# Optimization experiments

Hardware: AMD Instinct MI355X
Metric: run time of the kernel (lower is better)

## Reference

```python
import jax, jax.numpy as jnp
import numpy as np

DEPTH = 6


def sparsemax(z):
    # sparsemax along last axis (matches tfa.activations.sparsemax default axis=-1)
    d = z.shape[-1]
    z_sorted = -jnp.sort(-z, axis=-1)                      # descending
    cs = jnp.cumsum(z_sorted, axis=-1)
    k = jnp.arange(1, d + 1, dtype=z.dtype)
    support = z_sorted * k > (cs - 1.0)
    k_sup = jnp.sum(support, axis=-1, keepdims=True)       # size of support
    cs_k = jnp.take_along_axis(cs, k_sup.astype(jnp.int32) - 1, axis=-1)
    tau = (cs_k - 1.0) / k_sup.astype(z.dtype)
    return jnp.maximum(z - tau, 0.0)


def binary_lut(depth):
    # (depth, 2^depth, 2): bit s of each leaf code and its complement
    idx = jnp.arange(2 ** depth)
    off = 2 ** jnp.arange(depth)
    bits = (idx[None, :] // off[:, None]) % 2
    return jnp.stack([bits, 1 - bits], axis=-1).astype(jnp.float32)


def setup_inputs() -> dict:
    key = jax.random.key(0)
    ks = jax.random.split(key, 5)
    batch, dim, n_trees, depth, units = 1024, 256, 512, DEPTH, 16
    return {
        "x": jax.random.normal(ks[0], (batch, dim), dtype=jnp.float32),
        "feature_selection_logits": jax.random.normal(ks[1], (dim, n_trees, depth), dtype=jnp.float32),
        "feature_thresholds": jax.random.normal(ks[2], (n_trees, depth), dtype=jnp.float32) * 0.1,
        "log_temperatures": jax.random.normal(ks[3], (n_trees, depth), dtype=jnp.float32) * 0.1,
        "response": jax.random.normal(ks[4], (n_trees, units, 2 ** depth), dtype=jnp.float32),
    }


def reference(x, feature_selection_logits, feature_thresholds, log_temperatures, response):
    lut = binary_lut(DEPTH)                                     # (d, c, 2)
    selectors = sparsemax(feature_selection_logits)             # (i, n, d)
    fv = jnp.einsum('bi,ind->bnd', x, selectors)                # (b, n, d)
    tl = (fv - feature_thresholds) * jnp.exp(-log_temperatures) # (b, n, d)
    tl2 = jnp.stack([-tl, tl], axis=-1)                         # (b, n, d, 2)
    gates = jnp.clip(0.5 * tl2 + 0.5, 0.0, 1.0)                 # sparsemoid
    rg = jnp.einsum('bnds,dcs->bndc', gates, lut)               # (b, n, d, 2^d)
    rg = jnp.prod(rg, axis=-2)                                  # (b, n, 2^d)
    out = jnp.einsum('bnc,nuc->bnu', rg, response)              # (b, n, u)
    return jnp.mean(out, axis=1)                                # (b, u)
```

## Files before the change

kernel.cpp:

```cpp
#include <hip/hip_runtime.h>
#include <hip/hip_bf16.h>

#define DEPTH   6
#define NLEAF   64
#define BATCH   1024
#define DIM     256
#define NTREES  512
#define UNITS   16

#define BTILE   128
#define TTILE   8
#define KCHUNK  32
#define NTILES  (NTREES / TTILE)
#define BBLK    (BATCH / BTILE)
#define NDCOLS  (TTILE * DEPTH)

#define WS_SELP    0
#define WS_INVTEMP (WS_SELP + DIM*NTREES*DEPTH)
#define WS_THRP    (WS_INVTEMP + NTREES*DEPTH)
#define WS_PARTIAL (WS_THRP + NTREES*DEPTH)

__global__ void prep_small(const float* __restrict__ thr,
                           const float* __restrict__ lt,
                           float* __restrict__ invtemp,
                           float* __restrict__ thrp) {
    int i = blockIdx.x * 256 + threadIdx.x;
    if (i < NTREES * DEPTH) {
        float it = __expf(-lt[i]);
        invtemp[i] = it;
        thrp[i]    = thr[i] * it;
    }
}

__global__ void prep_sparsemax(const float* __restrict__ fsl,
                               const float* __restrict__ invtemp,
                               float* __restrict__ selp) {
    int t = blockIdx.x * 256 + threadIdx.x;
    int i = t >> 9;
    int n = t & (NTREES - 1);
    int base = (i * NTREES + n) * DEPTH;

    float zv[DEPTH], zs[DEPTH];
#pragma unroll
    for (int d = 0; d < DEPTH; ++d) { zv[d] = fsl[base + d]; zs[d] = zv[d]; }

#pragma unroll
    for (int p = 0; p < DEPTH - 1; ++p) {
#pragma unroll
        for (int j = 0; j < DEPTH - 1 - p; ++j) {
            float a = zs[j], b = zs[j + 1];
            zs[j]     = fmaxf(a, b);
            zs[j + 1] = fminf(a, b);
        }
    }

    float cs[DEPTH];
    cs[0] = zs[0];
#pragma unroll
    for (int d = 1; d < DEPTH; ++d) cs[d] = cs[d - 1] + zs[d];

    int k = 0;
#pragma unroll
    for (int d = 0; d < DEPTH; ++d)
        if (zs[d] * (float)(d + 1) > cs[d] - 1.0f) k++;

    float csk = cs[0];
#pragma unroll
    for (int d = 0; d < DEPTH; ++d) csk = (k - 1 == d) ? cs[d] : csk;

    float tau = (csk - 1.0f) / (float)k;

#pragma unroll
    for (int d = 0; d < DEPTH; ++d) {
        float it = invtemp[n * DEPTH + d];
        selp[base + d] = fmaxf(zv[d] - tau, 0.0f) * it;
    }
}

__global__ __launch_bounds__(256)
void main_kernel(const float* __restrict__ x,
                 const float* __restrict__ selp,
                 const float* __restrict__ thrp,
                 const float* __restrict__ resp,
                 float* __restrict__ partial) {
    __shared__ union SM {
        struct {
            float x[KCHUNK][132];
            float sel[KCHUNK][TTILE * 8];
        } a;
        float gates[NDCOLS][BTILE];
    } sm;

    const int tid   = threadIdx.x;
    const int ntile = blockIdx.x;
    const int btile = blockIdx.y;
    const int b0    = btile * BTILE;
    const int col0  = ntile * NDCOLS;
    const int ng0   = ntile * TTILE;

    const int tn = tid & (TTILE - 1);
    const int tb = tid >> 3;

    float acc[4][DEPTH];
#pragma unroll
    for (int bb = 0; bb < 4; ++bb)
#pragma unroll
        for (int d = 0; d < DEPTH; ++d) acc[bb][d] = 0.0f;

    for (int kc = 0; kc < DIM; kc += KCHUNK) {
#pragma unroll
        for (int i = 0; i < 16; ++i) {
            int e = tid + i * 256;
            int b = e >> 5;
            int k = e & 31;
            sm.a.x[k][b] = x[(b0 + b) * DIM + kc + k];
        }
#pragma unroll
        for (int i = 0; i < 6; ++i) {
            int e = tid + i * 256;
            int k = e / NDCOLS;
            int c = e - k * NDCOLS;
            int tt = c / DEPTH;
            int d  = c - tt * DEPTH;
            sm.a.sel[k][tt * 8 + d] = selp[(kc + k) * (NTREES * DEPTH) + col0 + c];
        }
        __syncthreads();

#pragma unroll 8
        for (int k = 0; k < KCHUNK; ++k) {
            float4 xv = *(const float4*)&sm.a.x[k][tb * 4];
            float4 s0 = *(const float4*)&sm.a.sel[k][tn * 8];
            float2 s1 = *(const float2*)&sm.a.sel[k][tn * 8 + 4];
            float xb[4] = {xv.x, xv.y, xv.z, xv.w};
            float sv[DEPTH] = {s0.x, s0.y, s0.z, s0.w, s1.x, s1.y};
#pragma unroll
            for (int bb = 0; bb < 4; ++bb)
#pragma unroll
                for (int d = 0; d < DEPTH; ++d)
                    acc[bb][d] = fmaf(xb[bb], sv[d], acc[bb][d]);
        }
        __syncthreads();
    }

#pragma unroll
    for (int d = 0; d < DEPTH; ++d) {
        float th = thrp[(ng0 + tn) * DEPTH + d];
#pragma unroll
        for (int bb = 0; bb < 4; ++bb) {
            float tl = acc[bb][d] - th;
            float g  = fminf(fmaxf(0.5f * tl + 0.5f, 0.0f), 1.0f);
            sm.gates[tn * DEPTH + d][tb * 4 + bb] = g;
        }
    }
    __syncthreads();

    const int b  = tid & (BTILE - 1);
    const int uh = __builtin_amdgcn_readfirstlane(tid >> 7);

    float out8[8];
#pragma unroll
    for (int u = 0; u < 8; ++u) out8[u] = 0.0f;

    for (int n = 0; n < TTILE; ++n) {
        float g[DEPTH];
#pragma unroll
        for (int d = 0; d < DEPTH; ++d) g[d] = sm.gates[n * DEPTH + d][b];

        float p[NLEAF];
        p[0] = 1.0f;
#pragma unroll
        for (int d = 0; d < DEPTH; ++d) {
            int w = 1 << d;
            float gd = g[d], hd = 1.0f - g[d];
#pragma unroll
            for (int c = w - 1; c >= 0; --c) {
                float base = p[c];
                p[c + w] = base * hd;
                p[c]     = base * gd;
            }
        }

        const float* rp = resp + (((ng0 + n) * UNITS) + uh * 8) * NLEAF;
#pragma unroll
        for (int u = 0; u < 8; ++u) {
            float a = 0.0f;
#pragma unroll
            for (int c = 0; c < NLEAF; ++c)
                a = fmaf(p[c], rp[u * NLEAF + c], a);
            out8[u] += a;
        }
    }

    float* pp = partial + ((size_t)(ntile * BATCH + b0 + b)) * UNITS + uh * 8;
    float4 w0 = {out8[0], out8[1], out8[2], out8[3]};
    float4 w1 = {out8[4], out8[5], out8[6], out8[7]};
    *(float4*)&pp[0] = w0;
    *(float4*)&pp[4] = w1;
}

__global__ void reduce_kernel(const float* __restrict__ partial,
                              float* __restrict__ out) {
    int idx = blockIdx.x * 256 + threadIdx.x;
    float s = 0.0f;
#pragma unroll 8
    for (int nt = 0; nt < NTILES; ++nt)
        s += partial[(size_t)nt * BATCH * UNITS + idx];
    out[idx] = s * (1.0f / (float)NTREES);
}

extern "C" void kernel_launch(void* const* d_in, const int* in_sizes, int n_in,
                              void* d_out, int out_size, void* d_ws, size_t ws_size,
                              hipStream_t stream) {
    const float* x    = (const float*)d_in[0];
    const float* fsl  = (const float*)d_in[1];
    const float* thr  = (const float*)d_in[2];
    const float* lt   = (const float*)d_in[3];
    const float* resp = (const float*)d_in[4];
    float* out = (float*)d_out;
    float* ws  = (float*)d_ws;

    float* selp    = ws + WS_SELP;
    float* invtemp = ws + WS_INVTEMP;
    float* thrp    = ws + WS_THRP;
    float* partial = ws + WS_PARTIAL;

    prep_small<<<(NTREES * DEPTH + 255) / 256, 256, 0, stream>>>(thr, lt, invtemp, thrp);
    prep_sparsemax<<<(DIM * NTREES) / 256, 256, 0, stream>>>(fsl, invtemp, selp);
    main_kernel<<<dim3(NTILES, BBLK), 256, 0, stream>>>(x, selp, thrp, resp, partial);
    reduce_kernel<<<(BATCH * UNITS) / 256, 256, 0, stream>>>(partial, out);
}
```

Measured before the change: 158.6 us.

## Split fused kernel into register-tiled GEMM for gates and separate tree kernel

Replaces the fused GEMM-plus-tree kernel with a dedicated 64x64 register-tiled GEMM that writes gates to a global buffer, followed by a tree kernel that processes four trees per thread straight from those gates. It also merges the two prep kernels into one and aliases the selector buffer with the partial-sum buffer. The aim is better GEMM efficiency and occupancy than the shared-memory-limited fused design, paid for by a 12 MB gates round-trip through global memory. The old fused path is kept as a fallback when the workspace is too small.

New measurement: 232.4 us. +46.5%, slower.

```diff
diff --git a/kernel.cpp b/kernel.cpp
--- a/kernel.cpp
+++ b/kernel.cpp
@@ -7,52 +7,59 @@
 #define DIM     256
 #define NTREES  512
 #define UNITS   16
-
-#define BTILE   128
-#define TTILE   8
-#define KCHUNK  32
-#define NTILES  (NTREES / TTILE)
-#define BBLK    (BATCH / BTILE)
-#define NDCOLS  (TTILE * DEPTH)
-
-#define WS_SELP    0
-#define WS_INVTEMP (WS_SELP + DIM*NTREES*DEPTH)
-#define WS_THRP    (WS_INVTEMP + NTREES*DEPTH)
-#define WS_PARTIAL (WS_THRP + NTREES*DEPTH)
-
-__global__ void prep_small(const float* __restrict__ thr,
-                           const float* __restrict__ lt,
-                           float* __restrict__ invtemp,
-                           float* __restrict__ thrp) {
-    int i = blockIdx.x * 256 + threadIdx.x;
-    if (i < NTREES * DEPTH) {
-        float it = __expf(-lt[i]);
-        invtemp[i] = it;
-        thrp[i]    = thr[i] * it;
-    }
-}
-
-__global__ void prep_sparsemax(const float* __restrict__ fsl,
-                               const float* __restrict__ invtemp,
-                               float* __restrict__ selp) {
+#define NCOLS   (NTREES*DEPTH)
+
+#define TM    64
+#define TN    64
+#define KCH   32
+#define APAD  36
+#define BPAD  68
+#define MB    (BATCH/TM)
+#define NB    (NCOLS/TN)
+
+#define TPT   4
+#define NTG   (NTREES/TPT)
+
+#define WS_GATES 0
+#define WS_THRP  (WS_GATES + BATCH*NCOLS)
+#define WS_SH    (WS_THRP + NCOLS)
+#define WS_PRIMARY_FLOATS (WS_SH + NTG*BATCH*UNITS)
+
+#define FB_SELP    0
+#define FB_THRP    (FB_SELP + DIM*NTREES*DEPTH)
+#define FB_PARTIAL (FB_THRP + NCOLS)
+#define FBT   8
+#define FBB   128
+#define FBK   32
+#define FBNT  (NTREES/FBT)
+#define FBBB  (BATCH/FBB)
+#define FBND  (FBT*DEPTH)
+
+__global__ void prep_kernel(const float* __restrict__ fsl,
+                            const float* __restrict__ thr,
+                            const float* __restrict__ lt,
+                            float* __restrict__ selp,
+                            float* __restrict__ thrp) {
+    if (blockIdx.x == (DIM * NTREES) / 256) {
+        for (int j = threadIdx.x; j < NCOLS; j += 256)
+            thrp[j] = thr[j] * __expf(-lt[j]);
+        return;
+    }
     int t = blockIdx.x * 256 + threadIdx.x;
-    int i = t >> 9;
     int n = t & (NTREES - 1);
-    int base = (i * NTREES + n) * DEPTH;
+    int base = t * DEPTH;
 
     float zv[DEPTH], zs[DEPTH];
 #pragma unroll
     for (int d = 0; d < DEPTH; ++d) { zv[d] = fsl[base + d]; zs[d] = zv[d]; }
 
 #pragma unroll
-    for (int p = 0; p < DEPTH - 1; ++p) {
+    for (int p = 0; p < DEPTH - 1; ++p)
 #pragma unroll
         for (int j = 0; j < DEPTH - 1 - p; ++j) {
             float a = zs[j], b = zs[j + 1];
-            zs[j]     = fmaxf(a, b);
-            zs[j + 1] = fminf(a, b);
-        }
-    }
+            zs[j] = fmaxf(a, b); zs[j + 1] = fminf(a, b);
+        }
 
     float cs[DEPTH];
     cs[0] = zs[0];
@@ -67,38 +74,196 @@
     float csk = cs[0];
 #pragma unroll
     for (int d = 0; d < DEPTH; ++d) csk = (k - 1 == d) ? cs[d] : csk;
-
     float tau = (csk - 1.0f) / (float)k;
 
 #pragma unroll
     for (int d = 0; d < DEPTH; ++d) {
-        float it = invtemp[n * DEPTH + d];
+        float it = __expf(-lt[n * DEPTH + d]);
         selp[base + d] = fmaxf(zv[d] - tau, 0.0f) * it;
     }
 }
 
+__global__ __launch_bounds__(128)
+void gemm_gates(const float* __restrict__ x,
+                const float* __restrict__ selp,
+                const float* __restrict__ thrp,
+                float* __restrict__ gates) {
+    __shared__ float la[TM * APAD];
+    __shared__ float lb[KCH * BPAD];
+
+    const int tid = threadIdx.x;
+    const int n0  = blockIdx.x * TN;
+    const int m0  = blockIdx.y * TM;
+    const int tx  = tid & 7;
+    const int ty  = tid >> 3;
+
+    float acc[4][8];
+#pragma unroll
+    for (int r = 0; r < 4; ++r)
+#pragma unroll
+        for (int c = 0; c < 8; ++c) acc[r][c] = 0.0f;
+
+    float4 ra[4], rb[4];
+    int ar[4], ak[4], bk[4], bc_[4];
+#pragma unroll
+    for (int i = 0; i < 4; ++i) {
+        int e = tid + i * 128;
+        ar[i] = e >> 3;  ak[i] = e & 7;
+        bk[i] = e >> 4;  bc_[i] = e & 15;
+    }
+
+#define STAGE(KC_)                                                            \
+    _Pragma("unroll")                                                         \
+    for (int i = 0; i < 4; ++i) {                                             \
+        ra[i] = *(const float4*)&x[(m0 + ar[i]) * DIM + (KC_) * KCH + ak[i] * 4]; \
+        rb[i] = *(const float4*)&selp[((KC_) * KCH + bk[i]) * NCOLS + n0 + bc_[i] * 4]; \
+    }
+#define COMMIT()                                                              \
+    _Pragma("unroll")                                                         \
+    for (int i = 0; i < 4; ++i) {                                             \
+        *(float4*)&la[ar[i] * APAD + ak[i] * 4] = ra[i];                      \
+        *(float4*)&lb[bk[i] * BPAD + bc_[i] * 4] = rb[i];                     \
+    }
+
+    STAGE(0)
+    COMMIT()
+    __syncthreads();
+
+    const int NKC = DIM / KCH;
+    for (int kc = 0; kc < NKC; ++kc) {
+        if (kc < NKC - 1) STAGE(kc + 1)
+
+#pragma unroll
+        for (int kk = 0; kk < KCH; kk += 4) {
+            float a4[4][4];
+#pragma unroll
+            for (int r = 0; r < 4; ++r)
+                *(float4*)a4[r] = *(const float4*)&la[(ty * 4 + r) * APAD + kk];
+            float b4[4][8];
+#pragma unroll
+            for (int j = 0; j < 4; ++j) {
+                *(float4*)&b4[j][0] = *(const float4*)&lb[(kk + j) * BPAD + tx * 8];
+                *(float4*)&b4[j][4] = *(const float4*)&lb[(kk + j) * BPAD + tx * 8 + 4];
+            }
+#pragma unroll
+            for (int j = 0; j < 4; ++j)
+#pragma unroll
+                for (int r = 0; r < 4; ++r)
+#pragma unroll
+                    for (int c = 0; c < 8; ++c)
+                        acc[r][c] = fmaf(a4[r][j], b4[j][c], acc[r][c]);
+        }
+
+        if (kc < NKC - 1) {
+            __syncthreads();
+            COMMIT()
+            __syncthreads();
+        }
+    }
+#undef STAGE
+#undef COMMIT
+
+    float th[8];
+    *(float4*)&th[0] = *(const float4*)&thrp[n0 + tx * 8];
+    *(float4*)&th[4] = *(const float4*)&thrp[n0 + tx * 8 + 4];
+#pragma unroll
+    for (int r = 0; r < 4; ++r) {
+        float o[8];
+#pragma unroll
+        for (int c = 0; c < 8; ++c) {
+            float tl = acc[r][c] - th[c];
+            o[c] = fminf(fmaxf(fmaf(0.5f, tl, 0.5f), 0.0f), 1.0f);
+        }
+        float* gp = &gates[(size_t)(m0 + ty * 4 + r) * NCOLS + n0 + tx * 8];
+        *(float4*)&gp[0] = *(float4*)&o[0];
+        *(float4*)&gp[4] = *(float4*)&o[4];
+    }
+}
+
 __global__ __launch_bounds__(256)
-void main_kernel(const float* __restrict__ x,
-                 const float* __restrict__ selp,
-                 const float* __restrict__ thrp,
+void tree_kernel(const float* __restrict__ gates,
                  const float* __restrict__ resp,
                  float* __restrict__ partial) {
+    const int bid  = blockIdx.x;
+    const int bc   = bid & 7;
+    const int tg   = bid >> 3;
+    const int tid  = threadIdx.x;
+    const int lane = tid & 63;
+    const int uh   = __builtin_amdgcn_readfirstlane((tid >> 6) & 1);
+    const int b    = bc * 128 + (tid >> 7) * 64 + lane;
+
+    float g[TPT * DEPTH];
+    const float* gp = gates + (size_t)b * NCOLS + tg * (TPT * DEPTH);
+#pragma unroll
+    for (int i = 0; i < 6; ++i)
+        *(float4*)&g[i * 4] = *(const float4*)&gp[i * 4];
+
+    float out8[8];
+#pragma unroll
+    for (int u = 0; u < 8; ++u) out8[u] = 0.0f;
+
+#pragma unroll
+    for (int t = 0; t < TPT; ++t) {
+        float p[NLEAF];
+        p[0] = 1.0f;
+#pragma unroll
+        for (int d = 0; d < DEPTH; ++d) {
+            int w = 1 << d;
+            float gd = g[t * DEPTH + d], hd = 1.0f - gd;
+#pragma unroll
+            for (int c = w - 1; c >= 0; --c) {
+                float base = p[c];
+                p[c + w] = base * hd;
+                p[c]     = base * gd;
+            }
+        }
+        const float* rp = resp + (size_t)((tg * TPT + t) * UNITS + uh * 8) * NLEAF;
+#pragma unroll
+        for (int u = 0; u < 8; ++u) {
+            float a = 0.0f;
+#pragma unroll
+            for (int c = 0; c < NLEAF; ++c)
+                a = fmaf(p[c], rp[u * NLEAF + c], a);
+            out8[u] += a;
+        }
+    }
+
+    float* pp = partial + ((size_t)tg * BATCH + b) * UNITS + uh * 8;
+    *(float4*)&pp[0] = *(float4*)&out8[0];
+    *(float4*)&pp[4] = *(float4*)&out8[4];
+}
+
+__global__ void reduce_kernel(const float* __restrict__ partial,
+                              float* __restrict__ out, int nt) {
+    int idx = blockIdx.x * 256 + threadIdx.x;
+    float s = 0.0f;
+    for (int tg = 0; tg < nt; ++tg)
+        s += partial[(size_t)tg * BATCH * UNITS + idx];
+    out[idx] = s * (1.0f / (float)NTREES);
+}
+
+__global__ __launch_bounds__(256)
+void fused_kernel(const float* __restrict__ x,
+                  const float* __restrict__ selp,
+                  const float* __restrict__ thrp,
+                  const float* __restrict__ resp,
+                  float* __restrict__ partial) {
     __shared__ union SM {
         struct {
-            float x[KCHUNK][132];
-            float sel[KCHUNK][TTILE * 8];
+            float x[FBK][132];
+            float sel[FBK][FBT * 8];
         } a;
-        float gates[NDCOLS][BTILE];
+        float gates[FBND][FBB];
     } sm;
 
     const int tid   = threadIdx.x;
     const int ntile = blockIdx.x;
     const int btile = blockIdx.y;
-    const int b0    = btile * BTILE;
-    const int col0  = ntile * NDCOLS;
-    const int ng0   = ntile * TTILE;
-
-    const int tn = tid & (TTILE - 1);
+    const int b0    = btile * FBB;
+    const int col0  = ntile * FBND;
+    const int ng0   = ntile * FBT;
+
+    const int tn = tid & (FBT - 1);
     const int tb = tid >> 3;
 
     float acc[4][DEPTH];
@@ -107,7 +272,7 @@
 #pragma unroll
         for (int d = 0; d < DEPTH; ++d) acc[bb][d] = 0.0f;
 
-    for (int kc = 0; kc < DIM; kc += KCHUNK) {
+    for (int kc = 0; kc < DIM; kc += FBK) {
 #pragma unroll
         for (int i = 0; i < 16; ++i) {
             int e = tid + i * 256;
@@ -118,16 +283,16 @@
 #pragma unroll
         for (int i = 0; i < 6; ++i) {
             int e = tid + i * 256;
-            int k = e / NDCOLS;
-            int c = e - k * NDCOLS;
+            int k = e / FBND;
+            int c = e - k * FBND;
             int tt = c / DEPTH;
             int d  = c - tt * DEPTH;
-            sm.a.sel[k][tt * 8 + d] = selp[(kc + k) * (NTREES * DEPTH) + col0 + c];
+            sm.a.sel[k][tt * 8 + d] = selp[(kc + k) * NCOLS + col0 + c];
         }
         __syncthreads();
 
 #pragma unroll 8
-        for (int k = 0; k < KCHUNK; ++k) {
+        for (int k = 0; k < FBK; ++k) {
             float4 xv = *(const float4*)&sm.a.x[k][tb * 4];
             float4 s0 = *(const float4*)&sm.a.sel[k][tn * 8];
             float2 s1 = *(const float2*)&sm.a.sel[k][tn * 8 + 4];
@@ -154,14 +319,14 @@
     }
     __syncthreads();
 
-    const int b  = tid & (BTILE - 1);
+    const int b  = tid & (FBB - 1);
     const int uh = __builtin_amdgcn_readfirstlane(tid >> 7);
 
     float out8[8];
 #pragma unroll
     for (int u = 0; u < 8; ++u) out8[u] = 0.0f;
 
-    for (int n = 0; n < TTILE; ++n) {
+    for (int n = 0; n < FBT; ++n) {
         float g[DEPTH];
 #pragma unroll
         for (int d = 0; d < DEPTH; ++d) g[d] = sm.gates[n * DEPTH + d][b];
@@ -192,20 +357,8 @@
     }
 
     float* pp = partial + ((size_t)(ntile * BATCH + b0 + b)) * UNITS + uh * 8;
-    float4 w0 = {out8[0], out8[1], out8[2], out8[3]};
-    float4 w1 = {out8[4], out8[5], out8[6], out8[7]};
-    *(float4*)&pp[0] = w0;
-    *(float4*)&pp[4] = w1;
-}
-
-__global__ void reduce_kernel(const float* __restrict__ partial,
-                              float* __restrict__ out) {
-    int idx = blockIdx.x * 256 + threadIdx.x;
-    float s = 0.0f;
-#pragma unroll 8
-    for (int nt = 0; nt < NTILES; ++nt)
-        s += partial[(size_t)nt * BATCH * UNITS + idx];
-    out[idx] = s * (1.0f / (float)NTREES);
+    *(float4*)&pp[0] = *(float4*)&out8[0];
+    *(float4*)&pp[4] = *(float4*)&out8[4];
 }
 
 extern "C" void kernel_launch(void* const* d_in, const int* in_sizes, int n_in,
@@ -219,13 +372,23 @@
     float* out = (float*)d_out;
     float* ws  = (float*)d_ws;
 
-    float* selp    = ws + WS_SELP;
-    float* invtemp = ws + WS_INVTEMP;
-    float* thrp    = ws + WS_THRP;
-    float* partial = ws + WS_PARTIAL;
-
-    prep_small<<<(NTREES * DEPTH + 255) / 256, 256, 0, stream>>>(thr, lt, invtemp, thrp);
-    prep_sparsemax<<<(DIM * NTREES) / 256, 256, 0, stream>>>(fsl, invtemp, selp);
-    main_kernel<<<dim3(NTILES, BBLK), 256, 0, stream>>>(x, selp, thrp, resp, partial);
-    reduce_kernel<<<(BATCH * UNITS) / 256, 256, 0, stream>>>(partial, out);
-}
+    if (ws_size >= (size_t)WS_PRIMARY_FLOATS * sizeof(float)) {
+        float* gates   = ws + WS_GATES;
+        float* thrp    = ws + WS_THRP;
+        float* selp    = ws + WS_SH;
+        float* partial = ws + WS_SH;
+
+        prep_kernel<<<(DIM * NTREES) / 256 + 1, 256, 0, stream>>>(fsl, thr, lt, selp, thrp);
+        gemm_gates<<<dim3(NB, MB), 128, 0, stream>>>(x, selp, thrp, gates);
+        tree_kernel<<<NTG * 8, 256, 0, stream>>>(gates, resp, partial);
+        reduce_kernel<<<(BATCH * UNITS) / 256, 256, 0, stream>>>(partial, out, NTG);
+    } else {
+        float* selp    = ws + FB_SELP;
+        float* thrp    = ws + FB_THRP;
+        float* partial = ws + FB_PARTIAL;
+
+        prep_kernel<<<(DIM * NTREES) / 256 + 1, 256, 0, stream>>>(fsl, thr, lt, selp, thrp);
+        fused_kernel<<<dim3(FBNT, FBBB), 256, 0, stream>>>(x, selp, thrp, resp, partial);
+        reduce_kernel<<<(BATCH * UNITS) / 256, 256, 0, stream>>>(partial, out, FBNT);
+    }
+}
```

## Split fused tree kernel into double-buffered GEMM for gates plus separate tree kernel

Applied to the files above, without the earlier changes.

Replaces the fused kernel, which did the projection and the tree evaluation together, with a standalone 64x64-tiled GEMM that uses double-buffered shared memory and float4 loads. That GEMM writes clipped gates to a workspace buffer, and a separate tree kernel then reads those gates straight from global memory. The intent is a more efficient GEMM with better operand reuse and latency hiding, plus smaller tree tiles (4 trees per block) for more parallelism. The two prep kernels are merged, and selp and partial share a workspace region. In exchange, a 12 MB gates buffer is written and read through global memory, and the reduce kernel now sums 128 partials instead of 64.

Measured after the change: 529.2 us. +233.7%, slower.

```diff
diff --git a/kernel.cpp b/kernel.cpp
--- a/kernel.cpp
+++ b/kernel.cpp
@@ -7,52 +7,49 @@
 #define DIM     256
 #define NTREES  512
 #define UNITS   16
-
-#define BTILE   128
-#define TTILE   8
-#define KCHUNK  32
-#define NTILES  (NTREES / TTILE)
-#define BBLK    (BATCH / BTILE)
-#define NDCOLS  (TTILE * DEPTH)
-
-#define WS_SELP    0
-#define WS_INVTEMP (WS_SELP + DIM*NTREES*DEPTH)
-#define WS_THRP    (WS_INVTEMP + NTREES*DEPTH)
-#define WS_PARTIAL (WS_THRP + NTREES*DEPTH)
-
-__global__ void prep_small(const float* __restrict__ thr,
-                           const float* __restrict__ lt,
-                           float* __restrict__ invtemp,
-                           float* __restrict__ thrp) {
-    int i = blockIdx.x * 256 + threadIdx.x;
-    if (i < NTREES * DEPTH) {
-        float it = __expf(-lt[i]);
-        invtemp[i] = it;
-        thrp[i]    = thr[i] * it;
-    }
-}
-
-__global__ void prep_sparsemax(const float* __restrict__ fsl,
-                               const float* __restrict__ invtemp,
-                               float* __restrict__ selp) {
+#define NCOLS   (NTREES*DEPTH)
+
+#define TM    64
+#define TN    64
+#define KCH   32
+#define APAD  36
+#define BPAD  68
+#define MB    (BATCH/TM)
+#define NB    (NCOLS/TN)
+#define NKC   (DIM/KCH)
+
+#define TPT   4
+#define NTG   (NTREES/TPT)
+
+#define WS_GATES 0
+#define WS_THRP  (WS_GATES + BATCH*NCOLS)
+#define WS_SH    (WS_THRP + NCOLS)
+
+__global__ void prep_kernel(const float* __restrict__ fsl,
+                            const float* __restrict__ thr,
+                            const float* __restrict__ lt,
+                            float* __restrict__ selp,
+                            float* __restrict__ thrp) {
+    if (blockIdx.x == (DIM * NTREES) / 256) {
+        for (int j = threadIdx.x; j < NCOLS; j += 256)
+            thrp[j] = thr[j] * __expf(-lt[j]);
+        return;
+    }
     int t = blockIdx.x * 256 + threadIdx.x;
-    int i = t >> 9;
     int n = t & (NTREES - 1);
-    int base = (i * NTREES + n) * DEPTH;
+    int base = t * DEPTH;
 
     float zv[DEPTH], zs[DEPTH];
 #pragma unroll
     for (int d = 0; d < DEPTH; ++d) { zv[d] = fsl[base + d]; zs[d] = zv[d]; }
 
 #pragma unroll
-    for (int p = 0; p < DEPTH - 1; ++p) {
+    for (int p = 0; p < DEPTH - 1; ++p)
 #pragma unroll
         for (int j = 0; j < DEPTH - 1 - p; ++j) {
             float a = zs[j], b = zs[j + 1];
-            zs[j]     = fmaxf(a, b);
-            zs[j + 1] = fminf(a, b);
-        }
-    }
+            zs[j] = fmaxf(a, b); zs[j + 1] = fminf(a, b);
+        }
 
     float cs[DEPTH];
     cs[0] = zs[0];
@@ -67,111 +64,130 @@
     float csk = cs[0];
 #pragma unroll
     for (int d = 0; d < DEPTH; ++d) csk = (k - 1 == d) ? cs[d] : csk;
-
     float tau = (csk - 1.0f) / (float)k;
 
 #pragma unroll
     for (int d = 0; d < DEPTH; ++d) {
-        float it = invtemp[n * DEPTH + d];
+        float it = __expf(-lt[n * DEPTH + d]);
         selp[base + d] = fmaxf(zv[d] - tau, 0.0f) * it;
     }
 }
 
-__global__ __launch_bounds__(256)
-void main_kernel(const float* __restrict__ x,
-                 const float* __restrict__ selp,
-                 const float* __restrict__ thrp,
+__global__ __launch_bounds__(256, 4)
+void gemm_gates(const float* __restrict__ x,
+                const float* __restrict__ selp,
+                const float* __restrict__ thrp,
+                float* __restrict__ gates) {
+    __shared__ float la[2][TM * APAD];
+    __shared__ float lb[2][KCH * BPAD];
+
+    const int tid = threadIdx.x;
+    const int n0  = blockIdx.x * TN;
+    const int m0  = blockIdx.y * TM;
+    const int tx  = tid & 15;
+    const int ty  = tid >> 4;
+
+    float acc[4][4];
+#pragma unroll
+    for (int r = 0; r < 4; ++r)
+#pragma unroll
+        for (int c = 0; c < 4; ++c) acc[r][c] = 0.0f;
+
+    float4 ra[2], rb[2];
+
+#define STAGE(KC_)                                                             \
+    _Pragma("unroll")                                                          \
+    for (int j = 0; j < 2; ++j) {                                              \
+        int f = tid + j * 256;                                                 \
+        ra[j] = *(const float4*)&x[(m0 + (f >> 3)) * DIM + (KC_) * KCH + (f & 7) * 4]; \
+        rb[j] = *(const float4*)&selp[((KC_) * KCH + (f >> 4)) * NCOLS + n0 + (f & 15) * 4]; \
+    }
+#define COMMIT(P_)                                                             \
+    _Pragma("unroll")                                                          \
+    for (int j = 0; j < 2; ++j) {                                              \
+        int f = tid + j * 256;                                                 \
+        *(float4*)&la[P_][(f >> 3) * APAD + (f & 7) * 4] = ra[j];              \
+        *(float4*)&lb[P_][(f >> 4) * BPAD + (f & 15) * 4] = rb[j];             \
+    }
+
+    STAGE(0)
+    COMMIT(0)
+    __syncthreads();
+
+    for (int kc = 0; kc < NKC; ++kc) {
+        const int par = kc & 1;
+        if (kc < NKC - 1) STAGE(kc + 1)
+
+#pragma unroll
+        for (int kk = 0; kk < KCH; kk += 4) {
+            float a4[4][4], b4[4][4];
+#pragma unroll
+            for (int r = 0; r < 4; ++r)
+                *(float4*)a4[r] = *(const float4*)&la[par][(ty * 4 + r) * APAD + kk];
+#pragma unroll
+            for (int j = 0; j < 4; ++j)
+                *(float4*)b4[j] = *(const float4*)&lb[par][(kk + j) * BPAD + tx * 4];
+#pragma unroll
+            for (int j = 0; j < 4; ++j)
+#pragma unroll
+                for (int r = 0; r < 4; ++r)
+#pragma unroll
+                    for (int c = 0; c < 4; ++c)
+                        acc[r][c] = fmaf(a4[r][j], b4[j][c], acc[r][c]);
+        }
+
+        if (kc < NKC - 1) {
+            COMMIT(par ^ 1)
+            __syncthreads();
+        }
+    }
+#undef STAGE
+#undef COMMIT
+
+    float4 th4 = *(const float4*)&thrp[n0 + tx * 4];
+    float th[4] = {th4.x, th4.y, th4.z, th4.w};
+#pragma unroll
+    for (int r = 0; r < 4; ++r) {
+        float o[4];
+#pragma unroll
+        for (int c = 0; c < 4; ++c) {
+            float tl = acc[r][c] - th[c];
+            o[c] = fminf(fmaxf(fmaf(0.5f, tl, 0.5f), 0.0f), 1.0f);
+        }
+        *(float4*)&gates[(size_t)(m0 + ty * 4 + r) * NCOLS + n0 + tx * 4] = *(float4*)&o[0];
+    }
+}
+
+__global__ __launch_bounds__(256, 4)
+void tree_kernel(const float* __restrict__ gates,
                  const float* __restrict__ resp,
                  float* __restrict__ partial) {
-    __shared__ union SM {
-        struct {
-            float x[KCHUNK][132];
-            float sel[KCHUNK][TTILE * 8];
-        } a;
-        float gates[NDCOLS][BTILE];
-    } sm;
-
-    const int tid   = threadIdx.x;
-    const int ntile = blockIdx.x;
-    const int btile = blockIdx.y;
-    const int b0    = btile * BTILE;
-    const int col0  = ntile * NDCOLS;
-    const int ng0   = ntile * TTILE;
-
-    const int tn = tid & (TTILE - 1);
-    const int tb = tid >> 3;
-
-    float acc[4][DEPTH];
-#pragma unroll
-    for (int bb = 0; bb < 4; ++bb)
-#pragma unroll
-        for (int d = 0; d < DEPTH; ++d) acc[bb][d] = 0.0f;
-
-    for (int kc = 0; kc < DIM; kc += KCHUNK) {
-#pragma unroll
-        for (int i = 0; i < 16; ++i) {
-            int e = tid + i * 256;
-            int b = e >> 5;
-            int k = e & 31;
-            sm.a.x[k][b] = x[(b0 + b) * DIM + kc + k];
-        }
-#pragma unroll
-        for (int i = 0; i < 6; ++i) {
-            int e = tid + i * 256;
-            int k = e / NDCOLS;
-            int c = e - k * NDCOLS;
-            int tt = c / DEPTH;
-            int d  = c - tt * DEPTH;
-            sm.a.sel[k][tt * 8 + d] = selp[(kc + k) * (NTREES * DEPTH) + col0 + c];
-        }
-        __syncthreads();
-
-#pragma unroll 8
-        for (int k = 0; k < KCHUNK; ++k) {
-            float4 xv = *(const float4*)&sm.a.x[k][tb * 4];
-            float4 s0 = *(const float4*)&sm.a.sel[k][tn * 8];
-            float2 s1 = *(const float2*)&sm.a.sel[k][tn * 8 + 4];
-            float xb[4] = {xv.x, xv.y, xv.z, xv.w};
-            float sv[DEPTH] = {s0.x, s0.y, s0.z, s0.w, s1.x, s1.y};
-#pragma unroll
-            for (int bb = 0; bb < 4; ++bb)
-#pragma unroll
-                for (int d = 0; d < DEPTH; ++d)
-                    acc[bb][d] = fmaf(xb[bb], sv[d], acc[bb][d]);
-        }
-        __syncthreads();
-    }
-
-#pragma unroll
-    for (int d = 0; d < DEPTH; ++d) {
-        float th = thrp[(ng0 + tn) * DEPTH + d];
-#pragma unroll
-        for (int bb = 0; bb < 4; ++bb) {
-            float tl = acc[bb][d] - th;
-            float g  = fminf(fmaxf(0.5f * tl + 0.5f, 0.0f), 1.0f);
-            sm.gates[tn * DEPTH + d][tb * 4 + bb] = g;
-        }
-    }
-    __syncthreads();
-
-    const int b  = tid & (BTILE - 1);
-    const int uh = __builtin_amdgcn_readfirstlane(tid >> 7);
+    const int bid  = blockIdx.x;
+    const int bc   = bid & 7;
+    const int tg   = bid >> 3;
+    const int tid  = threadIdx.x;
+    const int uh   = __builtin_amdgcn_readfirstlane((tid >> 6) & 1);
+    const int b    = bc * 128 + (tid >> 7) * 64 + (tid & 63);
+
+    const float* gp = gates + (size_t)b * NCOLS + tg * (TPT * DEPTH);
 
     float out8[8];
 #pragma unroll
     for (int u = 0; u < 8; ++u) out8[u] = 0.0f;
 
-    for (int n = 0; n < TTILE; ++n) {
+#pragma unroll
+    for (int t = 0; t < TPT; ++t) {
         float g[DEPTH];
 #pragma unroll
-        for (int d = 0; d < DEPTH; ++d) g[d] = sm.gates[n * DEPTH + d][b];
+        for (int i = 0; i < 3; ++i)
+            *(float2*)&g[i * 2] = *(const float2*)&gp[t * DEPTH + i * 2];
 
         float p[NLEAF];
         p[0] = 1.0f;
 #pragma unroll
         for (int d = 0; d < DEPTH; ++d) {
             int w = 1 << d;
-            float gd = g[d], hd = 1.0f - g[d];
+            float gd = g[d], hd = 1.0f - gd;
 #pragma unroll
             for (int c = w - 1; c >= 0; --c) {
                 float base = p[c];
@@ -180,31 +196,40 @@
             }
         }
 
-        const float* rp = resp + (((ng0 + n) * UNITS) + uh * 8) * NLEAF;
+        const float4* rp4 = (const float4*)(resp +
+            (size_t)((tg * TPT + t) * UNITS + uh * 8) * NLEAF);
 #pragma unroll
         for (int u = 0; u < 8; ++u) {
-            float a = 0.0f;
-#pragma unroll
-            for (int c = 0; c < NLEAF; ++c)
-                a = fmaf(p[c], rp[u * NLEAF + c], a);
-            out8[u] += a;
-        }
-    }
-
-    float* pp = partial + ((size_t)(ntile * BATCH + b0 + b)) * UNITS + uh * 8;
-    float4 w0 = {out8[0], out8[1], out8[2], out8[3]};
-    float4 w1 = {out8[4], out8[5], out8[6], out8[7]};
-    *(float4*)&pp[0] = w0;
-    *(float4*)&pp[4] = w1;
+            float s0 = 0.0f, s1 = 0.0f;
+#pragma unroll
+            for (int c4 = 0; c4 < 16; c4 += 2) {
+                float4 r0 = rp4[u * 16 + c4];
+                float4 r1 = rp4[u * 16 + c4 + 1];
+                s0 = fmaf(p[c4 * 4 + 0], r0.x, s0);
+                s0 = fmaf(p[c4 * 4 + 1], r0.y, s0);
+                s0 = fmaf(p[c4 * 4 + 2], r0.z, s0);
+                s0 = fmaf(p[c4 * 4 + 3], r0.w, s0);
+                s1 = fmaf(p[c4 * 4 + 4], r1.x, s1);
+                s1 = fmaf(p[c4 * 4 + 5], r1.y, s1);
+                s1 = fmaf(p[c4 * 4 + 6], r1.z, s1);
+                s1 = fmaf(p[c4 * 4 + 7], r1.w, s1);
+            }
+            out8[u] += s0 + s1;
+        }
+    }
+
+    float* pp = partial + ((size_t)tg * BATCH + b) * UNITS + uh * 8;
+    *(float4*)&pp[0] = *(float4*)&out8[0];
+    *(float4*)&pp[4] = *(float4*)&out8[4];
 }
 
 __global__ void reduce_kernel(const float* __restrict__ partial,
                               float* __restrict__ out) {
     int idx = blockIdx.x * 256 + threadIdx.x;
     float s = 0.0f;
-#pragma unroll 8
-    for (int nt = 0; nt < NTILES; ++nt)
-        s += partial[(size_t)nt * BATCH * UNITS + idx];
+#pragma unroll 16
+    for (int tg = 0; tg < NTG; ++tg)
+        s += partial[(size_t)tg * BATCH * UNITS + idx];
     out[idx] = s * (1.0f / (float)NTREES);
 }
 
@@ -219,13 +244,13 @@
     float* out = (float*)d_out;
     float* ws  = (float*)d_ws;
 
-    float* selp    = ws + WS_SELP;
-    float* invtemp = ws + WS_INVTEMP;
+    float* gates   = ws + WS_GATES;
     float* thrp    = ws + WS_THRP;
-    float* partial = ws + WS_PARTIAL;
-
-    prep_small<<<(NTREES * DEPTH + 255) / 256, 256, 0, stream>>>(thr, lt, invtemp, thrp);
-    prep_sparsemax<<<(DIM * NTREES) / 256, 256, 0, stream>>>(fsl, invtemp, selp);
-    main_kernel<<<dim3(NTILES, BBLK), 256, 0, stream>>>(x, selp, thrp, resp, partial);
+    float* selp    = ws + WS_SH;
+    float* partial = ws + WS_SH;
+
+    prep_kernel<<<(DIM * NTREES) / 256 + 1, 256, 0, stream>>>(fsl, thr, lt, selp, thrp);
+    gemm_gates<<<dim3(NB, MB), 256, 0, stream>>>(x, selp, thrp, gates);
+    tree_kernel<<<NTG * 8, 256, 0, stream>>>(gates, resp, partial);
     reduce_kernel<<<(BATCH * UNITS) / 256, 256, 0, stream>>>(partial, out);
 }
```
